# Performance work log

Measured on AMD Instinct MI355X. Metric: run time of the kernel, lower is better.

The kernel has to match this reference:

```python
import jax, jax.numpy as jnp
import numpy as np

EPS = 1e-12  # torch F.normalize eps

def setup_inputs() -> dict:
    key = jax.random.key(0)
    k1, k2, k3, k4 = jax.random.split(key, 4)
    bs, n_tok, in_dim = 64, 2048, 1024   # in_dim = 2*time_dim
    expert_dim, n_experts = 256, 512     # n_experts == 'channels' in the torch code
    x = jax.random.normal(k1, (bs, n_tok, in_dim), dtype=jnp.float32)
    W = jax.random.normal(k2, (expert_dim, in_dim), dtype=jnp.float32) * (1.0 / np.sqrt(in_dim))
    b = jax.random.normal(k3, (expert_dim,), dtype=jnp.float32) * 0.01
    centers = jax.random.normal(k4, (n_experts, expert_dim), dtype=jnp.float32)
    return {"x": x, "W": W, "b": b, "centers": centers, "top_k": 2}

def _l2norm(v):
    return v / jnp.maximum(jnp.linalg.norm(v, axis=-1, keepdims=True), EPS)

def reference(x, W, b, centers, top_k):
    # projection: (bs, n, in_dim) @ (in_dim, expert_dim)
    x_proj = jnp.einsum('bni,ei->bne', x, W) + b
    x_proj = _l2norm(x_proj)
    c = _l2norm(centers)                       # (n_experts, expert_dim)
    cosine_sim = jnp.einsum('bnd,ed->bne', x_proj, c)  # (bs, n, n_experts)
    topk_vals, topk_idx = jax.lax.top_k(cosine_sim, top_k)
    topk_probs = jax.nn.softmax(topk_vals, axis=-1)
    return topk_probs, topk_idx
```

## Files before the change

### kernel.cpp

```cpp
#include <hip/hip_runtime.h>
#include <math.h>

#define IN_DIM 1024
#define E_DIM  256
#define N_EXP  512
#define N_TOK  131072
#define TM     32
#define BK     32
#define XS_STR 36
#define WS_STR 36

typedef double d4 __attribute__((ext_vector_type(4)));

__device__ __forceinline__ void ins2(double v, int c,
                                     double& v1, int& i1, double& v2, int& i2)
{
    if (v > v1 || (v == v1 && c < i1)) { v2 = v1; i2 = i1; v1 = v; i1 = c; }
    else if (v > v2 || (v == v2 && c < i2)) { v2 = v; i2 = c; }
}

__global__ __launch_bounds__(64) void center_norm_kernel(
    const float* __restrict__ centers, double* __restrict__ cTd)
{
    const int ctr  = blockIdx.x;
    const int lane = threadIdx.x;
    const float* row = centers + (size_t)ctr * E_DIM;
    double v[4];
    double s = 0.0;
#pragma unroll
    for (int i = 0; i < 4; ++i) { v[i] = (double)row[lane + 64 * i]; s = fma(v[i], v[i], s); }
#pragma unroll
    for (int off = 32; off >= 1; off >>= 1) s += __shfl_xor(s, off, 64);
    const double inv = 1.0 / fmax(sqrt(s), 1e-12);
#pragma unroll
    for (int i = 0; i < 4; ++i)
        cTd[(size_t)(lane + 64 * i) * N_EXP + ctr] = v[i] * inv;
}

__global__ __launch_bounds__(256, 2) void router_kernel(
    const float* __restrict__ x, const float* __restrict__ W,
    const float* __restrict__ bias, const double* __restrict__ cTd,
    float* __restrict__ out)
{
    __shared__ __align__(16) char smem_raw[65536];
    const int tid  = threadIdx.x;
    const int lane = tid & 63;
    const int wv   = tid >> 6;
    const int r    = lane & 15;
    const int q    = lane >> 4;
    const int tokBase = blockIdx.x * TM;

    float* xs  = (float*)smem_raw;
    float* wsm = (float*)(smem_raw + TM * XS_STR * 4);

    d4 acc[2][4];
#pragma unroll
    for (int m = 0; m < 2; ++m)
#pragma unroll
        for (int n = 0; n < 4; ++n) acc[m][n] = (d4){0.0, 0.0, 0.0, 0.0};

    const int lt = tid >> 3;
    const int lk = (tid & 7) * 4;

    for (int k0 = 0; k0 < IN_DIM; k0 += BK) {
        {
            const float4 xv = *(const float4*)(x + (size_t)(tokBase + lt) * IN_DIM + k0 + lk);
            *(float4*)(xs + lt * XS_STR + lk) = xv;
        }
#pragma unroll
        for (int p = 0; p < 8; ++p) {
            const int e = lt + p * 32;
            const float4 wvv = *(const float4*)(W + (size_t)e * IN_DIM + k0 + lk);
            *(float4*)(wsm + e * WS_STR + lk) = wvv;
        }
        __syncthreads();
#pragma unroll
        for (int kk = 0; kk < 8; ++kk) {
            const int k = kk * 4 + q;
            const double a0 = (double)xs[r * XS_STR + k];
            const double a1 = (double)xs[(16 + r) * XS_STR + k];
#pragma unroll
            for (int n = 0; n < 4; ++n) {
                const double b = (double)wsm[(wv * 64 + n * 16 + r) * WS_STR + k];
                acc[0][n] = __builtin_amdgcn_mfma_f64_16x16x4f64(a0, b, acc[0][n], 0, 0, 0);
                acc[1][n] = __builtin_amdgcn_mfma_f64_16x16x4f64(a1, b, acc[1][n], 0, 0, 0);
            }
        }
        __syncthreads();
    }

#pragma unroll
    for (int n = 0; n < 4; ++n) {
        const double bb = (double)bias[wv * 64 + n * 16 + r];
#pragma unroll
        for (int m = 0; m < 2; ++m)
#pragma unroll
            for (int i = 0; i < 4; ++i) acc[m][n][i] += bb;
    }

    double* partials = (double*)smem_raw;
    double ss[2][4];
#pragma unroll
    for (int m = 0; m < 2; ++m)
#pragma unroll
        for (int i = 0; i < 4; ++i) {
            double s = 0.0;
#pragma unroll
            for (int n = 0; n < 4; ++n) s = fma(acc[m][n][i], acc[m][n][i], s);
#pragma unroll
            for (int off = 8; off >= 1; off >>= 1) s += __shfl_xor(s, off, 64);
            ss[m][i] = s;
        }
    if (r == 0) {
#pragma unroll
        for (int m = 0; m < 2; ++m)
#pragma unroll
            for (int i = 0; i < 4; ++i)
                partials[wv * 32 + m * 16 + q * 4 + i] = ss[m][i];
    }
    __syncthreads();

    double inv[2][4];
#pragma unroll
    for (int m = 0; m < 2; ++m)
#pragma unroll
        for (int i = 0; i < 4; ++i) {
            const int t = m * 16 + q * 4 + i;
            const double s = partials[t] + partials[32 + t] + partials[64 + t] + partials[96 + t];
            inv[m][i] = 1.0 / fmax(sqrt(s), 1e-12);
        }
    __syncthreads();

    double* projn = (double*)smem_raw;
#pragma unroll
    for (int m = 0; m < 2; ++m)
#pragma unroll
        for (int n = 0; n < 4; ++n)
#pragma unroll
            for (int i = 0; i < 4; ++i)
                projn[(wv * 64 + n * 16 + r) * 32 + m * 16 + q * 4 + i] = acc[m][n][i] * inv[m][i];
    __syncthreads();

    double tv1[2][4], tv2[2][4];
    int    ti1[2][4], ti2[2][4];
#pragma unroll
    for (int m = 0; m < 2; ++m)
#pragma unroll
        for (int i = 0; i < 4; ++i) {
            tv1[m][i] = -1e300; tv2[m][i] = -1e300; ti1[m][i] = 0; ti2[m][i] = 0;
        }

    for (int pass = 0; pass < 2; ++pass) {
        const int colbase = wv * 128 + pass * 64;
        d4 acc2[2][4];
#pragma unroll
        for (int m = 0; m < 2; ++m)
#pragma unroll
            for (int n = 0; n < 4; ++n) acc2[m][n] = (d4){0.0, 0.0, 0.0, 0.0};

        const double* cb = cTd + colbase + r;
#pragma unroll 4
        for (int kk = 0; kk < 64; ++kk) {
            const int k = kk * 4 + q;
            const double a0 = projn[k * 32 + r];
            const double a1 = projn[k * 32 + 16 + r];
#pragma unroll
            for (int n = 0; n < 4; ++n) {
                const double b = cb[(size_t)k * N_EXP + n * 16];
                acc2[0][n] = __builtin_amdgcn_mfma_f64_16x16x4f64(a0, b, acc2[0][n], 0, 0, 0);
                acc2[1][n] = __builtin_amdgcn_mfma_f64_16x16x4f64(a1, b, acc2[1][n], 0, 0, 0);
            }
        }
#pragma unroll
        for (int m = 0; m < 2; ++m)
#pragma unroll
            for (int i = 0; i < 4; ++i)
#pragma unroll
                for (int n = 0; n < 4; ++n)
                    ins2(acc2[m][n][i], colbase + n * 16 + r,
                         tv1[m][i], ti1[m][i], tv2[m][i], ti2[m][i]);
    }

#pragma unroll
    for (int m = 0; m < 2; ++m)
#pragma unroll
        for (int i = 0; i < 4; ++i) {
#pragma unroll
            for (int off = 8; off >= 1; off >>= 1) {
                const double ov1 = __shfl_xor(tv1[m][i], off, 64);
                const int    oi1 = __shfl_xor(ti1[m][i], off, 64);
                const double ov2 = __shfl_xor(tv2[m][i], off, 64);
                const int    oi2 = __shfl_xor(ti2[m][i], off, 64);
                ins2(ov1, oi1, tv1[m][i], ti1[m][i], tv2[m][i], ti2[m][i]);
                ins2(ov2, oi2, tv1[m][i], ti1[m][i], tv2[m][i], ti2[m][i]);
            }
        }

    __syncthreads();
    double* cand = (double*)smem_raw;
    if (r == 0) {
#pragma unroll
        for (int m = 0; m < 2; ++m)
#pragma unroll
            for (int i = 0; i < 4; ++i) {
                const int t = m * 16 + q * 4 + i;
                double* cd = cand + ((wv * 32 + t) << 2);
                cd[0] = tv1[m][i]; cd[1] = (double)ti1[m][i];
                cd[2] = tv2[m][i]; cd[3] = (double)ti2[m][i];
            }
    }
    __syncthreads();

    if (tid < 32) {
        double v1 = -1e300, v2 = -1e300;
        int    i1 = 0, i2 = 0;
        for (int s = 0; s < 4; ++s) {
            const double* cd = cand + ((s * 32 + tid) << 2);
            ins2(cd[0], (int)cd[1], v1, i1, v2, i2);
            ins2(cd[2], (int)cd[3], v1, i1, v2, i2);
        }
        const double e  = exp(v2 - v1);
        const double dn = 1.0 + e;
        const size_t g  = (size_t)tokBase + tid;
        out[g * 2 + 0] = (float)(1.0 / dn);
        out[g * 2 + 1] = (float)(e / dn);
        out[(size_t)2 * N_TOK + g * 2 + 0] = (float)i1;
        out[(size_t)2 * N_TOK + g * 2 + 1] = (float)i2;
    }
}

extern "C" void kernel_launch(void* const* d_in, const int* in_sizes, int n_in,
                              void* d_out, int out_size, void* d_ws, size_t ws_size,
                              hipStream_t stream)
{
    const float* x       = (const float*)d_in[0];
    const float* W       = (const float*)d_in[1];
    const float* bias    = (const float*)d_in[2];
    const float* centers = (const float*)d_in[3];
    double* cTd = (double*)d_ws;
    float*  out = (float*)d_out;

    center_norm_kernel<<<N_EXP, 64, 0, stream>>>(centers, cTd);
    router_kernel<<<N_TOK / TM, 256, 0, stream>>>(x, W, bias, cTd, out);
}
```

Baseline: 2.881 ms.

## Register-prefetch next K tile in projection GEMM and narrow cosine passes

The projection GEMM loop now loads the next x/W tile from global memory into registers while the MFMAs on the current shared-memory tile run. This is meant to hide global load latency, at the cost of more registers for the prefetch buffers. The cosine-similarity stage is split into four passes of 32 columns instead of two of 64, with pointer-increment addressing and deeper unrolling. That lowers accumulator register pressure but reads the projection data from LDS twice as many times.

Result: slower. 3.414 ms (+18.5%).

```diff
diff --git a/kernel.cpp b/kernel.cpp
--- a/kernel.cpp
+++ b/kernel.cpp
@@ -62,18 +62,30 @@
     const int lt = tid >> 3;
     const int lk = (tid & 7) * 4;
 
+    const float* xp = x + (size_t)(tokBase + lt) * IN_DIM + lk;
+    const float* wp = W + (size_t)lt * IN_DIM + lk;
+
+    float4 xv = *(const float4*)xp;
+    float4 wreg[8];
+#pragma unroll
+    for (int p = 0; p < 8; ++p)
+        wreg[p] = *(const float4*)(wp + (size_t)(p * 32) * IN_DIM);
+
     for (int k0 = 0; k0 < IN_DIM; k0 += BK) {
-        {
-            const float4 xv = *(const float4*)(x + (size_t)(tokBase + lt) * IN_DIM + k0 + lk);
-            *(float4*)(xs + lt * XS_STR + lk) = xv;
-        }
-#pragma unroll
-        for (int p = 0; p < 8; ++p) {
-            const int e = lt + p * 32;
-            const float4 wvv = *(const float4*)(W + (size_t)e * IN_DIM + k0 + lk);
-            *(float4*)(wsm + e * WS_STR + lk) = wvv;
-        }
         __syncthreads();
+        *(float4*)(xs + lt * XS_STR + lk) = xv;
+#pragma unroll
+        for (int p = 0; p < 8; ++p)
+            *(float4*)(wsm + (lt + p * 32) * WS_STR + lk) = wreg[p];
+        __syncthreads();
+
+        if (k0 + BK < IN_DIM) {
+            xv = *(const float4*)(xp + k0 + BK);
+#pragma unroll
+            for (int p = 0; p < 8; ++p)
+                wreg[p] = *(const float4*)(wp + (size_t)(p * 32) * IN_DIM + k0 + BK);
+        }
+
 #pragma unroll
         for (int kk = 0; kk < 8; ++kk) {
             const int k = kk * 4 + q;
@@ -86,8 +98,8 @@
                 acc[1][n] = __builtin_amdgcn_mfma_f64_16x16x4f64(a1, b, acc[1][n], 0, 0, 0);
             }
         }
-        __syncthreads();
-    }
+    }
+    __syncthreads();
 
 #pragma unroll
     for (int n = 0; n < 4; ++n) {
@@ -150,33 +162,35 @@
             tv1[m][i] = -1e300; tv2[m][i] = -1e300; ti1[m][i] = 0; ti2[m][i] = 0;
         }
 
-    for (int pass = 0; pass < 2; ++pass) {
-        const int colbase = wv * 128 + pass * 64;
-        d4 acc2[2][4];
-#pragma unroll
-        for (int m = 0; m < 2; ++m)
-#pragma unroll
-            for (int n = 0; n < 4; ++n) acc2[m][n] = (d4){0.0, 0.0, 0.0, 0.0};
-
-        const double* cb = cTd + colbase + r;
-#pragma unroll 4
+    for (int pass = 0; pass < 4; ++pass) {
+        const int colbase = wv * 128 + pass * 32;
+        d4 acc2[2][2];
+#pragma unroll
+        for (int m = 0; m < 2; ++m)
+#pragma unroll
+            for (int n = 0; n < 2; ++n) acc2[m][n] = (d4){0.0, 0.0, 0.0, 0.0};
+
+        const double* cb = cTd + (size_t)q * N_EXP + colbase + r;
+        const double* pa = projn + q * 32 + r;
+#pragma unroll 8
         for (int kk = 0; kk < 64; ++kk) {
-            const int k = kk * 4 + q;
-            const double a0 = projn[k * 32 + r];
-            const double a1 = projn[k * 32 + 16 + r];
-#pragma unroll
-            for (int n = 0; n < 4; ++n) {
-                const double b = cb[(size_t)k * N_EXP + n * 16];
-                acc2[0][n] = __builtin_amdgcn_mfma_f64_16x16x4f64(a0, b, acc2[0][n], 0, 0, 0);
-                acc2[1][n] = __builtin_amdgcn_mfma_f64_16x16x4f64(a1, b, acc2[1][n], 0, 0, 0);
-            }
+            const double a0 = pa[0];
+            const double a1 = pa[16];
+            const double b0 = cb[0];
+            const double b1 = cb[16];
+            acc2[0][0] = __builtin_amdgcn_mfma_f64_16x16x4f64(a0, b0, acc2[0][0], 0, 0, 0);
+            acc2[1][0] = __builtin_amdgcn_mfma_f64_16x16x4f64(a1, b0, acc2[1][0], 0, 0, 0);
+            acc2[0][1] = __builtin_amdgcn_mfma_f64_16x16x4f64(a0, b1, acc2[0][1], 0, 0, 0);
+            acc2[1][1] = __builtin_amdgcn_mfma_f64_16x16x4f64(a1, b1, acc2[1][1], 0, 0, 0);
+            pa += 4 * 32;
+            cb += (size_t)4 * N_EXP;
         }
 #pragma unroll
         for (int m = 0; m < 2; ++m)
 #pragma unroll
             for (int i = 0; i < 4; ++i)
 #pragma unroll
-                for (int n = 0; n < 4; ++n)
+                for (int n = 0; n < 2; ++n)
                     ins2(acc2[m][n][i], colbase + n * 16 + r,
                          tv1[m][i], ti1[m][i], tv2[m][i], ti2[m][i]);
     }
```

## Double-buffer projection GEMM with direct global-to-LDS loads and XOR swizzle

Applied to the files above, without the earlier changes.

The projection GEMM main loop now uses global_load_lds to stream x and W tiles straight into LDS. Two buffers let the next K-slice load overlap the MFMA work on the current one, with one barrier per iteration instead of two. The K tile shrinks to 16 and the LDS layout uses an XOR swizzle in place of padding to avoid bank conflicts. This adds reliance on the async-load ordering semantics and more loop iterations.

After: 2.718 ms. 1.06x faster.

```diff
diff --git a/kernel.cpp b/kernel.cpp
--- a/kernel.cpp
+++ b/kernel.cpp
@@ -6,9 +6,9 @@
 #define N_EXP  512
 #define N_TOK  131072
 #define TM     32
-#define BK     32
-#define XS_STR 36
-#define WS_STR 36
+#define BK     16
+#define NT     64
+#define BUF_BYTES 18432
 
 typedef double d4 __attribute__((ext_vector_type(4)));
 
@@ -17,6 +17,14 @@
 {
     if (v > v1 || (v == v1 && c < i1)) { v2 = v1; i2 = i1; v1 = v; i1 = c; }
     else if (v > v2 || (v == v2 && c < i2)) { v2 = v; i2 = c; }
+}
+
+__device__ __forceinline__ void gload_lds16(const float* g, float* l)
+{
+    __builtin_amdgcn_global_load_lds(
+        (const __attribute__((address_space(1))) unsigned int*)(g),
+        (__attribute__((address_space(3))) unsigned int*)(l),
+        16, 0, 0);
 }
 
 __global__ __launch_bounds__(64) void center_norm_kernel(
@@ -50,8 +58,10 @@
     const int q    = lane >> 4;
     const int tokBase = blockIdx.x * TM;
 
-    float* xs  = (float*)smem_raw;
-    float* wsm = (float*)(smem_raw + TM * XS_STR * 4);
+    const int srow = lane >> 2;
+    const int scol = (lane & 3) ^ ((lane >> 3) & 3);
+    const float* xg = x + (size_t)(tokBase + (wv & 1) * 16 + srow) * IN_DIM + scol * 4;
+    const float* wg = W + (size_t)(wv * 16 + srow) * IN_DIM + scol * 4;
 
     d4 acc[2][4];
 #pragma unroll
@@ -59,34 +69,45 @@
 #pragma unroll
         for (int n = 0; n < 4; ++n) acc[m][n] = (d4){0.0, 0.0, 0.0, 0.0};
 
-    const int lt = tid >> 3;
-    const int lk = (tid & 7) * 4;
-
-    for (int k0 = 0; k0 < IN_DIM; k0 += BK) {
-        {
-            const float4 xv = *(const float4*)(x + (size_t)(tokBase + lt) * IN_DIM + k0 + lk);
-            *(float4*)(xs + lt * XS_STR + lk) = xv;
-        }
-#pragma unroll
-        for (int p = 0; p < 8; ++p) {
-            const int e = lt + p * 32;
-            const float4 wvv = *(const float4*)(W + (size_t)e * IN_DIM + k0 + lk);
-            *(float4*)(wsm + e * WS_STR + lk) = wvv;
-        }
-        __syncthreads();
-#pragma unroll
-        for (int kk = 0; kk < 8; ++kk) {
-            const int k = kk * 4 + q;
-            const double a0 = (double)xs[r * XS_STR + k];
-            const double a1 = (double)xs[(16 + r) * XS_STR + k];
+    const int swz   = (r >> 1) & 3;
+    const int abase = r * 16 + q;
+    const int bbase = (wv * 64 + r) * 16 + q;
+
+    {
+        float* b = (float*)smem_raw;
+        if (wv < 2) gload_lds16(xg, b + wv * 256);
+#pragma unroll
+        for (int p = 0; p < 4; ++p)
+            gload_lds16(wg + (size_t)p * 64 * IN_DIM, b + 512 + p * 1024 + wv * 256);
+    }
+    __syncthreads();
+
+    int cur = 0;
+    for (int t = 0; t < NT; ++t) {
+        if (t + 1 < NT) {
+            float* b = (float*)(smem_raw + (cur ^ 1) * BUF_BYTES);
+            const int k0 = (t + 1) * BK;
+            if (wv < 2) gload_lds16(xg + k0, b + wv * 256);
+#pragma unroll
+            for (int p = 0; p < 4; ++p)
+                gload_lds16(wg + (size_t)p * 64 * IN_DIM + k0, b + 512 + p * 1024 + wv * 256);
+        }
+        const float* xb = (const float*)(smem_raw + cur * BUF_BYTES);
+        const float* wb = xb + 512;
+#pragma unroll
+        for (int kk = 0; kk < 4; ++kk) {
+            const int so = 4 * (kk ^ swz);
+            const double a0 = (double)xb[abase + so];
+            const double a1 = (double)xb[abase + 256 + so];
 #pragma unroll
             for (int n = 0; n < 4; ++n) {
-                const double b = (double)wsm[(wv * 64 + n * 16 + r) * WS_STR + k];
+                const double b = (double)wb[bbase + n * 256 + so];
                 acc[0][n] = __builtin_amdgcn_mfma_f64_16x16x4f64(a0, b, acc[0][n], 0, 0, 0);
                 acc[1][n] = __builtin_amdgcn_mfma_f64_16x16x4f64(a1, b, acc[1][n], 0, 0, 0);
             }
         }
         __syncthreads();
+        cur ^= 1;
     }
 
 #pragma unroll
```
